# Optimization experiments

Hardware: AMD Instinct MI355X
Metric: run time of the kernel (lower is better)

Reference implementation:

```python
import jax, jax.numpy as jnp
import numpy as np
import math

D, H = 128, 8
B, LC, LQ = 8, 512, 64


def pos_signal(channels, length):
    # tensor2tensor timing signal, returned as [C, L]
    pos = jnp.arange(length, dtype=jnp.float32)
    nts = channels // 2
    inc = math.log(1.0e4) / (nts - 1)
    inv = jnp.exp(jnp.arange(nts, dtype=jnp.float32) * -inc)
    st = pos[:, None] * inv[None, :]                      # [L, nts]
    sig = jnp.concatenate([jnp.sin(st), jnp.cos(st)], 1)  # [L, C]
    return sig.T


def mask_logits(t, m):
    return t * m + (1.0 - m) * -1e30


def ln_c(x, g, b):  # LayerNorm over channel dim of [B, D, L]
    mu = jnp.mean(x, axis=1, keepdims=True)
    var = jnp.mean((x - mu) ** 2, axis=1, keepdims=True)
    return (x - mu) / jnp.sqrt(var + 1e-5) * g[None, :, None] + b[None, :, None]


def conv1x1(x, w, b=None):  # x [B, I, L], w [O, I]
    y = jnp.einsum('oi,bil->bol', w, x)
    return y if b is None else y + b[None, :, None]


def dw_sep_conv(x, dw, pw, pwb):  # depthwise (k, no bias) -> pointwise (bias) -> relu
    k = dw.shape[-1]
    y = jax.lax.conv_general_dilated(x, dw[:, None, :], (1,), [(k // 2, k // 2)],
        dimension_numbers=('NCH', 'OIH', 'NCH'), feature_group_count=x.shape[1])
    return jax.nn.relu(conv1x1(y, pw, pwb))


def self_attention(x, mem_w, q_w, mask, n_head):  # x [B, D, L]
    b, d, L = x.shape
    dh = d // n_head
    mem = jnp.einsum('oi,bil->blo', mem_w, x)  # [B, L, 2D]
    q = jnp.einsum('oi,bil->blo', q_w, x)      # [B, L, D]
    def heads(t):
        return t.reshape(b, L, n_head, dh).transpose(0, 2, 1, 3)  # [B, H, L, dh]
    Qh = heads(q) * dh ** -0.5
    K = heads(mem[..., :d])
    V = heads(mem[..., d:])
    logits = jnp.einsum('bhqe,bhke->bhqk', Qh, K)
    logits = mask_logits(logits, mask[:, None, None, :])
    w = jax.nn.softmax(logits, axis=-1)
    o = jnp.einsum('bhqk,bhke->bhqe', w, V)
    return o.transpose(0, 2, 1, 3).reshape(b, L, d).transpose(0, 2, 1)


def encoder_block(x, mask, p, n_head):
    out = x + pos_signal(x.shape[1], x.shape[2])[None]
    n_conv = p['dw'].shape[0]
    for i in range(n_conv):
        res = out
        out = ln_c(out, p['lnc_g'][i], p['lnc_b'][i])
        out = dw_sep_conv(out, p['dw'][i], p['pw'][i], p['pw_b'][i]) + res
    res = out
    out = ln_c(out, p['ln1_g'], p['ln1_b'])
    out = self_attention(out, p['mem_w'], p['q_w'], mask, n_head) + res
    res = out
    out = ln_c(out, p['ln2_g'], p['ln2_b'])
    out = jax.nn.relu(conv1x1(out, p['ffn1_w'], p['ffn1_b']))
    out = conv1x1(out, p['ffn2_w'], p['ffn2_b'])
    return out + res


def cq_attention(Ce, Qe, cmask, qmask, w4C, w4Q, w4mlu, cq_b):
    Cx = Ce.transpose(0, 2, 1)   # [B, Lc, 2D]
    Qx = Qe.transpose(0, 2, 1)   # [B, Lq, 2D]
    s0 = jnp.einsum('bld,d->bl', Cx, w4C)[:, :, None]
    s1 = jnp.einsum('bqd,d->bq', Qx, w4Q)[:, None, :]
    s2 = jnp.einsum('bld,bqd->blq', Cx * w4mlu[None, None, :], Qx)
    S = s0 + s1 + s2 + cq_b
    S1 = jax.nn.softmax(mask_logits(S, qmask[:, None, :]), axis=2)
    S2 = jax.nn.softmax(mask_logits(S, cmask[:, :, None]), axis=1)
    A = jnp.einsum('blq,bqd->bld', S1, Qx)
    Bt = jnp.einsum('blq,bmq,bmd->bld', S1, S2, Cx)  # (S1 @ S2^T) @ C
    out = jnp.concatenate([Cx, A, Cx * A, Cx * Bt], axis=2)
    return out.transpose(0, 2, 1)  # [B, 8D, Lc]


def _forward(C, Q, maskC, maskQ, e_dw, e_pw, e_pw_b, e_lnc_g, e_lnc_b, e_mem_w, e_q_w,
             e_ffn1_w, e_ffn1_b, e_ffn2_w, e_ffn2_b, e_ln1_g, e_ln1_b, e_ln2_g, e_ln2_b,
             w4C, w4Q, w4mlu, cq_b, resizer_w,
             m_dw, m_pw, m_pw_b, m_lnc_g, m_lnc_b, m_mem_w, m_q_w,
             m_ffn1_w, m_ffn1_b, m_ffn2_w, m_ffn2_b, m_ln1_g, m_ln1_b, m_ln2_g, m_ln2_b):
    ep = dict(dw=e_dw, pw=e_pw, pw_b=e_pw_b, lnc_g=e_lnc_g, lnc_b=e_lnc_b,
              mem_w=e_mem_w, q_w=e_q_w, ffn1_w=e_ffn1_w, ffn1_b=e_ffn1_b,
              ffn2_w=e_ffn2_w, ffn2_b=e_ffn2_b, ln1_g=e_ln1_g, ln1_b=e_ln1_b,
              ln2_g=e_ln2_g, ln2_b=e_ln2_b)
    mp = dict(dw=m_dw, pw=m_pw, pw_b=m_pw_b, lnc_g=m_lnc_g, lnc_b=m_lnc_b,
              mem_w=m_mem_w, q_w=m_q_w, ffn1_w=m_ffn1_w, ffn1_b=m_ffn1_b,
              ffn2_w=m_ffn2_w, ffn2_b=m_ffn2_b, ln1_g=m_ln1_g, ln1_b=m_ln1_b,
              ln2_g=m_ln2_g, ln2_b=m_ln2_b)
    Ce = encoder_block(C, maskC, ep, H)
    Qe = encoder_block(Q, maskQ, ep, H)
    Ce = jnp.concatenate([Ce, C], axis=1)  # encode_fusion -> [B, 2D, Lc]
    Qe = jnp.concatenate([Qe, Q], axis=1)
    X = cq_attention(Ce, Qe, maskC, maskQ, w4C, w4Q, w4mlu, cq_b)
    X = jnp.concatenate([X, Ce], axis=1)   # match_fusion -> [B, 10D, Lc]
    M0 = conv1x1(X, resizer_w)             # [B, D, Lc]

    def run(m):
        def step(carry, p):
            return encoder_block(carry, maskC, p, H), None
        m, _ = jax.lax.scan(step, m, mp)
        return m

    M1 = run(M0)
    M2 = run(M1)
    M3 = run(M2)
    return M1, M2, M3


def setup_inputs() -> dict:
    key = jax.random.key(0)
    ks = iter(jax.random.split(key, 48))
    def rn(shape, scale):
        return jax.random.normal(next(ks), shape, dtype=jnp.float32) * scale
    s1 = 1.0 / math.sqrt(D)
    s2 = 1.0 / math.sqrt(2 * D)
    f32 = jnp.float32
    return dict(
        C=rn((B, D, LC), 1.0), Q=rn((B, D, LQ), 1.0),
        maskC=jnp.ones((B, LC), f32), maskQ=jnp.ones((B, LQ), f32),
        e_dw=rn((4, D, 7), 1.0 / math.sqrt(7)), e_pw=rn((4, D, D), s1),
        e_pw_b=jnp.zeros((4, D), f32), e_lnc_g=jnp.ones((4, D), f32), e_lnc_b=jnp.zeros((4, D), f32),
        e_mem_w=rn((2 * D, D), s1), e_q_w=rn((D, D), s1),
        e_ffn1_w=rn((D, D), s1), e_ffn1_b=jnp.zeros((D,), f32),
        e_ffn2_w=rn((D, D), s1), e_ffn2_b=jnp.zeros((D,), f32),
        e_ln1_g=jnp.ones((D,), f32), e_ln1_b=jnp.zeros((D,), f32),
        e_ln2_g=jnp.ones((D,), f32), e_ln2_b=jnp.zeros((D,), f32),
        w4C=rn((2 * D,), s2), w4Q=rn((2 * D,), s2), w4mlu=rn((2 * D,), s2),
        cq_b=jnp.zeros((1,), f32),
        resizer_w=rn((D, 10 * D), 1.0 / math.sqrt(10 * D)),
        m_dw=rn((7, 2, D, 5), 1.0 / math.sqrt(5)), m_pw=rn((7, 2, D, D), s1),
        m_pw_b=jnp.zeros((7, 2, D), f32), m_lnc_g=jnp.ones((7, 2, D), f32), m_lnc_b=jnp.zeros((7, 2, D), f32),
        m_mem_w=rn((7, 2 * D, D), s1), m_q_w=rn((7, D, D), s1),
        m_ffn1_w=rn((7, D, D), s1), m_ffn1_b=jnp.zeros((7, D), f32),
        m_ffn2_w=rn((7, D, D), s1), m_ffn2_b=jnp.zeros((7, D), f32),
        m_ln1_g=jnp.ones((7, D), f32), m_ln1_b=jnp.zeros((7, D), f32),
        m_ln2_g=jnp.ones((7, D), f32), m_ln2_b=jnp.zeros((7, D), f32),
    )


def reference(C, Q, maskC, maskQ, e_dw, e_pw, e_pw_b, e_lnc_g, e_lnc_b, e_mem_w, e_q_w,
              e_ffn1_w, e_ffn1_b, e_ffn2_w, e_ffn2_b, e_ln1_g, e_ln1_b, e_ln2_g, e_ln2_b,
              w4C, w4Q, w4mlu, cq_b, resizer_w,
              m_dw, m_pw, m_pw_b, m_lnc_g, m_lnc_b, m_mem_w, m_q_w,
              m_ffn1_w, m_ffn1_b, m_ffn2_w, m_ffn2_b, m_ln1_g, m_ln1_b, m_ln2_g, m_ln2_b):
    return _forward(C, Q, maskC, maskQ, e_dw, e_pw, e_pw_b, e_lnc_g, e_lnc_b, e_mem_w, e_q_w,
                    e_ffn1_w, e_ffn1_b, e_ffn2_w, e_ffn2_b, e_ln1_g, e_ln1_b, e_ln2_g, e_ln2_b,
                    w4C, w4Q, w4mlu, cq_b, resizer_w,
                    m_dw, m_pw, m_pw_b, m_lnc_g, m_lnc_b, m_mem_w, m_q_w,
                    m_ffn1_w, m_ffn1_b, m_ffn2_w, m_ffn2_b, m_ln1_g, m_ln1_b, m_ln2_g, m_ln2_b)
```

## Files before the change

kernel.cpp:

```cpp
#include <hip/hip_runtime.h>
#include <math.h>

#define D_  128
#define B_  8
#define H_  8
#define LC_ 512
#define LQ_ 64

typedef float f32x4 __attribute__((ext_vector_type(4)));
typedef short bf16x8 __attribute__((ext_vector_type(8)));
typedef short short4v __attribute__((ext_vector_type(4)));
typedef unsigned short ushortT;

__device__ inline short bfr(float x) {
  unsigned u = __float_as_uint(x);
  u += 0x7fff + ((u >> 16) & 1);
  return (short)(u >> 16);
}
__device__ inline float bfi(ushortT u) {
  return __uint_as_float(((unsigned)u) << 16);
}

__device__ inline bf16x8 mk8(short4v lo, short4v hi) {
  bf16x8 r;
  r[0] = lo[0]; r[1] = lo[1]; r[2] = lo[2]; r[3] = lo[3];
  r[4] = hi[0]; r[5] = hi[1]; r[6] = hi[2]; r[7] = hi[3];
  return r;
}

__device__ inline bf16x8 ldA(const ushortT* row, int koff) {
  short4v lo = *(const short4v*)(row + koff);
  short4v hi = *(const short4v*)(row + koff + 16);
  return mk8(lo, hi);
}
__device__ inline bf16x8 ldB2(const ushortT* plo, const ushortT* phi) {
  short4v lo = *(const short4v*)plo;
  short4v hi = *(const short4v*)phi;
  return mk8(lo, hi);
}

__global__ void k_prep(const float* a0, const float* a1, const float* a2,
                       const float* a3, const float* a4, const float* a5,
                       const float* a6, const float* a7, const float* a8,
                       const float* a9, const float* a10, ushortT* dst) {
  int i = blockIdx.x * 256 + threadIdx.x;
  if (i >= 1114112) return;
  const float* s; int lo;
  if      (i <   65536) { s = a0;  lo = i; }
  else if (i <   98304) { s = a1;  lo = i - 65536; }
  else if (i <  114688) { s = a2;  lo = i - 98304; }
  else if (i <  131072) { s = a3;  lo = i - 114688; }
  else if (i <  147456) { s = a4;  lo = i - 131072; }
  else if (i <  311296) { s = a5;  lo = i - 147456; }
  else if (i <  540672) { s = a6;  lo = i - 311296; }
  else if (i <  770048) { s = a7;  lo = i - 540672; }
  else if (i <  884736) { s = a8;  lo = i - 770048; }
  else if (i <  999424) { s = a9;  lo = i - 884736; }
  else                  { s = a10; lo = i - 999424; }
  dst[i] = (ushortT)bfr(s[lo]);
}

template <int KK, int ADDPOS>
__global__ __launch_bounds__(256) void k_fusedconv(
    const float* __restrict__ x, float* __restrict__ yout,
    const float* __restrict__ dw1, const ushortT* __restrict__ pw1,
    const float* __restrict__ pb1, const float* __restrict__ g1,
    const float* __restrict__ be1,
    const float* __restrict__ dw2, const ushortT* __restrict__ pw2,
    const float* __restrict__ pb2, const float* __restrict__ g2w,
    const float* __restrict__ be2, int L) {
  const int HALO = KK / 2;
  const int W1 = 32 + 2 * HALO;
  __shared__ __align__(16) float raw[128 * 40];
  __shared__ __align__(16) ushortT l1o[128 * 36];
  __shared__ __align__(16) ushortT xbf1[32 * 32 * 4];
  __shared__ float mu1[40], rs1[40], mu2[32], rs2[32], ps[160], psq[160];
  ushortT* xbf2 = (ushortT*)raw;
  int l0 = blockIdx.x * 16;
  int o0 = blockIdx.y * 64;
  int b = blockIdx.z;
  int tid = threadIdx.x;
  for (int idx = tid; idx < 128 * W1; idx += 256) {
    int d = idx / W1, c = idx - d * W1;
    int gl = l0 - 8 - HALO + c;
    float v = 0.f;
    if (gl >= 0 && gl < L) {
      v = x[((size_t)b * 128 + d) * L + gl];
      if (ADDPOS) {
        int j = d & 63;
        float arg = (float)gl * expf(-(float)j * 0.14619588f);
        v += (d < 64) ? sinf(arg) : cosf(arg);
      }
    }
    raw[d * 40 + c] = v;
  }
  __syncthreads();
  if (tid < 4 * W1) {
    int c = tid % W1, hh = tid / W1;
    float s = 0.f, s2 = 0.f;
    for (int d = hh * 32; d < hh * 32 + 32; d++) {
      float v = raw[d * 40 + c];
      s += v; s2 += v * v;
    }
    ps[tid] = s; psq[tid] = s2;
  }
  __syncthreads();
  if (tid < W1) {
    float s = ps[tid] + ps[tid + W1] + ps[tid + 2 * W1] + ps[tid + 3 * W1];
    float s2 = psq[tid] + psq[tid + W1] + psq[tid + 2 * W1] + psq[tid + 3 * W1];
    float mu = s * (1.f / 128.f);
    float var = fmaxf(s2 * (1.f / 128.f) - mu * mu, 0.f);
    mu1[tid] = mu; rs1[tid] = rsqrtf(var + 1e-5f);
  }
  __syncthreads();
  {
    int cc0 = tid & 31, dbase = tid >> 5;
#pragma unroll
    for (int kq = 0; kq < 4; kq++) {
      short4v pk;
#pragma unroll
      for (int e = 0; e < 4; e++) {
        int d = dbase * 16 + kq * 4 + e;
        float gg = g1[d], bb = be1[d];
        const float* wr = dw1 + d * KK;
        float acc = 0.f;
#pragma unroll
        for (int t = 0; t < KK; t++) {
          int ci = cc0 + t;
          int gl = l0 - 8 - HALO + ci;
          float lv = 0.f;
          if (gl >= 0 && gl < L)
            lv = (raw[d * 40 + ci] - mu1[ci]) * rs1[ci] * gg + bb;
          acc += wr[t] * lv;
        }
        pk[e] = bfr(acc);
      }
      *(short4v*)&xbf1[(((dbase * 4 + kq) * 32) + cc0) * 4] = pk;
    }
  }
  __syncthreads();
  int w = tid >> 6, lane = tid & 63, g2 = lane >> 4, r = lane & 15;
  {
    f32x4 acc[2][2];
#pragma unroll
    for (int i = 0; i < 2; i++)
#pragma unroll
      for (int nt = 0; nt < 2; nt++) acc[i][nt] = (f32x4){0.f, 0.f, 0.f, 0.f};
#pragma unroll
    for (int i = 0; i < 2; i++) {
      const ushortT* arow = pw1 + (size_t)((2 * w + i) * 16 + r) * 128;
#pragma unroll
      for (int kk = 0; kk < 4; kk++) {
        bf16x8 a = ldA(arow, kk * 32 + g2 * 4);
#pragma unroll
// ... 318 lines not shown
  int b = blockIdx.z;
  int tid = threadIdx.x;
  int w = tid >> 6;
  int h = w & 7, kh = w >> 3;
  int lane = tid & 63;
  int g2 = lane >> 4, r = lane & 15;
  const float* qb = qp + ((size_t)b * 128 + h * 16) * L;
  const float* kb = memKV + ((size_t)b * 256 + h * 16) * L;
  const float* vb = memKV + ((size_t)b * 256 + 128 + h * 16) * L;
  const float* mk = mask + (size_t)b * L;
  int qcol = q0 + r;
  bf16x8 qf;
#pragma unroll
  for (int j = 0; j < 4; j++)
    qf[j] = bfr(qb[(size_t)(g2 * 4 + j) * L + qcol] * 0.25f);
  qf[4] = 0; qf[5] = 0; qf[6] = 0; qf[7] = 0;
  float m_run = -INFINITY, ssum = 0.f;
  f32x4 O = {0.f, 0.f, 0.f, 0.f};
  int kbeg = kh * (L / 2), kend = (kh + 1) * (L / 2);
  for (int k0 = kbeg; k0 < kend; k0 += NCH * 16) {
    f32x4 sd[NCH];
#pragma unroll
    for (int mc = 0; mc < NCH; mc++) {
      bf16x8 kf;
      int krow = k0 + mc * 16 + r;
#pragma unroll
      for (int j = 0; j < 4; j++)
        kf[j] = bfr(kb[(size_t)(g2 * 4 + j) * L + krow]);
      kf[4] = 0; kf[5] = 0; kf[6] = 0; kf[7] = 0;
      f32x4 z = {0.f, 0.f, 0.f, 0.f};
      sd[mc] = __builtin_amdgcn_mfma_f32_16x16x32_bf16(kf, qf, z, 0, 0, 0);
    }
    float tm = -INFINITY;
#pragma unroll
    for (int mc = 0; mc < NCH; mc++) {
#pragma unroll
      for (int p = 0; p < 4; p++) {
        float mv = mk[k0 + mc * 16 + g2 * 4 + p];
        float sv = sd[mc][p] * mv + (1.f - mv) * (-1e30f);
        sd[mc][p] = sv;
        tm = fmaxf(tm, sv);
      }
    }
    tm = fmaxf(tm, __shfl_xor(tm, 16));
    tm = fmaxf(tm, __shfl_xor(tm, 32));
    float nm = fmaxf(m_run, tm);
    float c = __expf(m_run - nm);
    ssum *= c;
    O[0] *= c; O[1] *= c; O[2] *= c; O[3] *= c;
    float psum = 0.f;
    bf16x8 pf[NCH / 2];
#pragma unroll
    for (int c2 = 0; c2 < NCH / 2; c2++) {
#pragma unroll
      for (int j = 0; j < 4; j++) {
        float e0 = __expf(sd[2 * c2][j] - nm);
        float e1 = __expf(sd[2 * c2 + 1][j] - nm);
        psum += e0 + e1;
        pf[c2][j] = bfr(e0);
        pf[c2][j + 4] = bfr(e1);
      }
    }
    psum += __shfl_xor(psum, 16);
    psum += __shfl_xor(psum, 32);
    ssum += psum;
#pragma unroll
    for (int c2 = 0; c2 < NCH / 2; c2++) {
      const float* vrow = vb + (size_t)r * L + k0 + c2 * 32 + g2 * 4;
      float4 v0 = *(const float4*)vrow;
      float4 v1 = *(const float4*)(vrow + 16);
      bf16x8 vf;
      vf[0] = bfr(v0.x); vf[1] = bfr(v0.y); vf[2] = bfr(v0.z); vf[3] = bfr(v0.w);
      vf[4] = bfr(v1.x); vf[5] = bfr(v1.y); vf[6] = bfr(v1.z); vf[7] = bfr(v1.w);
      O = __builtin_amdgcn_mfma_f32_16x16x32_bf16(vf, pf[c2], O, 0, 0, 0);
    }
    m_run = nm;
  }
  if (kh == 1) {
    msh[h][lane] = m_run;
    ssh[h][lane] = ssum;
#pragma unroll
    for (int p = 0; p < 4; p++) Osh[h][lane][p] = O[p];
  }
  __syncthreads();
  if (kh == 0) {
    float mB = msh[h][lane], sB = ssh[h][lane];
    float nm = fmaxf(m_run, mB);
    float cA = __expf(m_run - nm), cB = __expf(mB - nm);
    float inv = 1.f / (ssum * cA + sB * cB);
#pragma unroll
    for (int p = 0; p < 4; p++) {
      int d = h * 16 + g2 * 4 + p;
      float ov = (O[p] * cA + Osh[h][lane][p] * cB) * inv;
      updT[d * 16 + r] = cur[((size_t)b * 128 + d) * L + qcol] + ov;
    }
  }
  __syncthreads();
  {
    int c = tid & 15, hh = tid >> 4;
    float s = 0.f, s2 = 0.f;
    for (int d = hh * 2; d < hh * 2 + 2; d++) {
      float v = updT[d * 16 + c];
      s += v; s2 += v * v;
    }
    ps[tid] = s; psq[tid] = s2;
  }
  __syncthreads();
  if (tid < 16) {
    float s = 0.f, s2 = 0.f;
    for (int hh = 0; hh < 64; hh++) { s += ps[hh * 16 + tid]; s2 += psq[hh * 16 + tid]; }
    float mu = s * (1.f / 128.f);
    float var = fmaxf(s2 * (1.f / 128.f) - mu * mu, 0.f);
    mu_s[tid] = mu; rs_s[tid] = rsqrtf(var + 1e-5f);
  }
  __syncthreads();
  for (int idx = tid; idx < 2048; idx += 1024) {
    int d = idx >> 4, c = idx & 15;
    float val = (updT[d * 16 + c] - mu_s[c]) * rs_s[c] * g[d] + be[d];
    xbf[(((d >> 2) * 16) + c) * 4 + (d & 3)] = (ushortT)bfr(val);
  }
  __syncthreads();
  if (w < 8) {
    f32x4 acc = {0.f, 0.f, 0.f, 0.f};
    const ushortT* ar = w1bf + (size_t)(16 * w + r) * 128;
#pragma unroll
    for (int kk = 0; kk < 4; kk++) {
      bf16x8 a = ldA(ar, kk * 32 + g2 * 4);
      bf16x8 bb = ldB2(&xbf[(((kk * 8 + g2) * 16) + r) * 4],
                       &xbf[(((kk * 8 + 4 + g2) * 16) + r) * 4]);
      acc = __builtin_amdgcn_mfma_f32_16x16x32_bf16(a, bb, acc, 0, 0, 0);
    }
#pragma unroll
    for (int p = 0; p < 4; p++) {
      int dmid = 16 * w + g2 * 4 + p;
      float val = fmaxf(acc[p] + b1[dmid], 0.f);
      midbf[(((4 * w + g2) * 16) + r) * 4 + p] = (ushortT)bfr(val);
    }
  }
  __syncthreads();
  if (w < 8) {
    f32x4 a2 = {0.f, 0.f, 0.f, 0.f};
    const ushortT* ar = w2bf + (size_t)(16 * w + r) * 128;
#pragma unroll
    for (int kk = 0; kk < 4; kk++) {
      bf16x8 a = ldA(ar, kk * 32 + g2 * 4);
      bf16x8 bb = ldB2(&midbf[(((kk * 8 + g2) * 16) + r) * 4],
                       &midbf[(((kk * 8 + 4 + g2) * 16) + r) * 4]);
      a2 = __builtin_amdgcn_mfma_f32_16x16x32_bf16(a, bb, a2, 0, 0, 0);
    }
#pragma unroll
    for (int p = 0; p < 4; p++) {
      int o = 16 * w + g2 * 4 + p;
      cur[((size_t)b * 128 + o) * L + q0 + r] = a2[p] + b2[o] + updT[o * 16 + r];
    }
  }
}


__global__ void k_concat2(const float* __restrict__ x1, const float* __restrict__ x2,
                          float* __restrict__ out, int L, int total) {
  int idx = blockIdx.x * 256 + threadIdx.x;
  if (idx >= total) return;
  int l = idx % L;
  int c = (idx / L) & 255;
  int b = idx / (L * 256);
  float v = (c < 128) ? x1[((size_t)b * 128 + c) * L + l]
                      : x2[((size_t)b * 128 + (c - 128)) * L + l];
  out[idx] = v;
}

__global__ void k_cqSrow(const float* __restrict__ Ce, const float* __restrict__ Qe,
                         const float* __restrict__ w4C, const float* __restrict__ w4Q,
                         const float* __restrict__ w4mlu, const float* __restrict__ cqb,
                         const float* __restrict__ qmask,
                         float* __restrict__ S, float* __restrict__ S1) {
  int idx = blockIdx.x * 256 + threadIdx.x;
  int q = idx & 63;
  int l = (idx >> 6) % LC_;
  int b = (idx >> 6) / LC_;
  const float* ce = Ce + (size_t)b * 256 * LC_ + l;
  const float* qe = Qe + (size_t)b * 256 * LQ_ + q;
  float acc = 0.f, a0 = 0.f, a1 = 0.f;
#pragma unroll 8
  for (int j = 0; j < 256; j++) {
    float cv = ce[(size_t)j * LC_];
    float qv = qe[(size_t)j * LQ_];
    acc += cv * w4mlu[j] * qv;
    a0 += cv * w4C[j];
    a1 += qv * w4Q[j];
  }
  float sv = acc + a0 + a1 + cqb[0];
  S[idx] = sv;
  float mv = qmask[b * LQ_ + q];
  float v = sv * mv + (1.f - mv) * (-1e30f);
  float mx = v;
  for (int off = 32; off; off >>= 1) mx = fmaxf(mx, __shfl_xor(mx, off));
  float p = expf(v - mx);
  float s = p;
  for (int off = 32; off; off >>= 1) s += __shfl_xor(s, off);
  S1[idx] = p / s;
}

__global__ __launch_bounds__(256) void k_softmax_col(
    const float* __restrict__ S, const float* __restrict__ cmask, float* __restrict__ S2) {
  int q = blockIdx.x & 63, b = blockIdx.x >> 6;
  int tid = threadIdx.x;
  __shared__ float redm[4], reds[4];
  const float* col = S + (size_t)b * LC_ * LQ_ + q;
  const float* mk = cmask + b * LC_;
  float vm[2];
#pragma unroll
  for (int k = 0; k < 2; k++) {
    int l = tid + 256 * k;
    float mv = mk[l];
    vm[k] = col[(size_t)l * LQ_] * mv + (1.f - mv) * (-1e30f);
  }
  float mx = fmaxf(vm[0], vm[1]);
  for (int off = 32; off; off >>= 1) mx = fmaxf(mx, __shfl_xor(mx, off));
  if ((tid & 63) == 0) redm[tid >> 6] = mx;
  __syncthreads();
  mx = fmaxf(fmaxf(redm[0], redm[1]), fmaxf(redm[2], redm[3]));
  float e0 = expf(vm[0] - mx), e1 = expf(vm[1] - mx);
  float s = e0 + e1;
  for (int off = 32; off; off >>= 1) s += __shfl_xor(s, off);
  if ((tid & 63) == 0) reds[tid >> 6] = s;
  __syncthreads();
  float invs = 1.f / (reds[0] + reds[1] + reds[2] + reds[3]);
  float* out = S2 + (size_t)b * LC_ * LQ_ + q;
  out[(size_t)tid * LQ_] = e0 * invs;
  out[(size_t)(tid + 256) * LQ_] = e1 * invs;
}

__global__ void k_cqY(const float* __restrict__ S2, const float* __restrict__ Ce,
                      float* __restrict__ Y) {
  int idx = blockIdx.x * 256 + threadIdx.x;
  if (idx >= B_ * 256 * LQ_) return;
  int q = idx & 63;
  int j = (idx >> 6) & 255;
  int b = idx >> 14;
  const float* s2 = S2 + (size_t)b * LC_ * LQ_ + q;
  const float* ce = Ce + ((size_t)b * 256 + j) * LC_;
  float acc = 0.f;
#pragma unroll 8
  for (int l = 0; l < LC_; l++) acc += s2[(size_t)l * LQ_] * ce[l];
  Y[idx] = acc;
}

__global__ __launch_bounds__(256) void k_cqAB(
    const float* __restrict__ S1, const float* __restrict__ Qe, const float* __restrict__ Y,
    float* __restrict__ A, float* __restrict__ Bt) {
  __shared__ float s1s[64][65];
  int l0 = blockIdx.x * 64;
  int b = blockIdx.z;
  int tid = threadIdx.x;
  for (int idx = tid; idx < 64 * 64; idx += 256) {
    int l = idx >> 6, q = idx & 63;
    s1s[l][q] = S1[((size_t)b * LC_ + l0 + l) * LQ_ + q];
  }
  __syncthreads();
  int ll = tid & 63, jj = tid >> 6;
  int j = blockIdx.y * 4 + jj;
  const float* qe = Qe + ((size_t)b * 256 + j) * LQ_;
  const float* yb = Y + ((size_t)b * 256 + j) * LQ_;
  float a = 0.f, bt = 0.f;
#pragma unroll 8
  for (int q = 0; q < 64; q++) {
    float sv = s1s[ll][q];
    a += sv * qe[q];
    bt += sv * yb[q];
  }
  A[((size_t)b * 256 + j) * LC_ + l0 + ll] = a;
  Bt[((size_t)b * 256 + j) * LC_ + l0 + ll] = bt;
}

__global__ __launch_bounds__(256) void k_resizer_mfma(
    const float* __restrict__ Ce, const float* __restrict__ A,
    const float* __restrict__ Bt, const ushortT* __restrict__ wbf,
    float* __restrict__ y) {
  __shared__ __align__(16) ushortT xbf[16 * 16 * 4];
  int l0 = blockIdx.x * 16;
  int o0 = blockIdx.y * 64;
  int b = blockIdx.z;
  int tid = threadIdx.x;
  int w = tid >> 6, lane = tid & 63, g2 = lane >> 4, r = lane & 15;
  const ushortT* arow = wbf + (size_t)(o0 + 16 * w + r) * 1280;
  f32x4 acc0 = {0.f, 0.f, 0.f, 0.f};
  for (int kt = 0; kt < 1280; kt += 64) {
    __syncthreads();
    for (int idx = tid; idx < 1024; idx += 256) {
      int kloc = idx >> 4, cc = idx & 15;
      int ch = kt + kloc;
      int seg = ch >> 8;
      int j = ch & 255;
      size_t p = ((size_t)b * 256 + j) * LC_ + l0 + cc;
      float v;
      if (seg == 0 || seg == 4) v = Ce[p];
      else if (seg == 1) v = A[p];
      else if (seg == 2) v = Ce[p] * A[p];
      else v = Ce[p] * Bt[p];
      xbf[(((kloc >> 2) * 16) + cc) * 4 + (kloc & 3)] = (ushortT)bfr(v);
    }
    __syncthreads();
#pragma unroll
    for (int kk2 = 0; kk2 < 2; kk2++) {
      bf16x8 a = ldA(arow, kt + kk2 * 32 + g2 * 4);
      bf16x8 b0 = ldB2(&xbf[(((kk2 * 8 + g2) * 16) + r) * 4],
// ... 14 lines not shown
  const float* lnc_g[4]; const float* lnc_b[4];
  const float* dw[4]; const ushortT* pw[4]; const float* pw_b[4];
  const ushortT* mem_w; const ushortT* q_w;
  const float* ln1_g; const float* ln1_b;
  const ushortT* ffn1_w; const float* ffn1_b;
  const ushortT* ffn2_w; const float* ffn2_b;
  const float* ln2_g; const float* ln2_b;
};

static void conv_pair_only(hipStream_t st, const float* in, float* out, int L,
                           const BlkP& P, int i0, bool addpos) {
  dim3 gc(L / 16, 2, B_);
  if (addpos)
    k_fusedconv<7, 1><<<gc, 256, 0, st>>>(in, out,
        P.dw[i0], P.pw[i0], P.pw_b[i0], P.lnc_g[i0], P.lnc_b[i0],
        P.dw[i0+1], P.pw[i0+1], P.pw_b[i0+1], P.lnc_g[i0+1], P.lnc_b[i0+1], L);
  else
    k_fusedconv<7, 0><<<gc, 256, 0, st>>>(in, out,
        P.dw[i0], P.pw[i0], P.pw_b[i0], P.lnc_g[i0], P.lnc_b[i0],
        P.dw[i0+1], P.pw[i0+1], P.pw_b[i0+1], P.lnc_g[i0+1], P.lnc_b[i0+1], L);
}

template <int KK, int ADDPOS>
static void convproj(hipStream_t st, const float* in, float* out, float* mkv,
                     float* qpb, int L, const BlkP& P, int i0) {
  k_convproj<KK, ADDPOS><<<dim3(L / 16, 1, B_), 512, 0, st>>>(in, out,
      P.dw[i0], P.pw[i0], P.pw_b[i0], P.lnc_g[i0], P.lnc_b[i0],
      P.dw[i0+1], P.pw[i0+1], P.pw_b[i0+1], P.lnc_g[i0+1], P.lnc_b[i0+1],
      P.mem_w, P.q_w, P.ln1_g, P.ln1_b, mkv, qpb, L);
}

static void attnffn(hipStream_t st, float* cur, float* mkv, float* qpb,
                    const float* mask, int L, const BlkP& P) {
  if (L == LC_)
    k_attnffn<8><<<dim3(L / 16, 1, B_), 1024, 0, st>>>(mkv, qpb, mask, cur,
        P.ffn1_w, P.ffn1_b, P.ffn2_w, P.ffn2_b, P.ln2_g, P.ln2_b, L);
  else
    k_attnffn<2><<<dim3(L / 16, 1, B_), 1024, 0, st>>>(mkv, qpb, mask, cur,
        P.ffn1_w, P.ffn1_b, P.ffn2_w, P.ffn2_b, P.ln2_g, P.ln2_b, L);
}

extern "C" void kernel_launch(void* const* d_in, const int* in_sizes, int n_in,
                              void* d_out, int out_size, void* d_ws, size_t ws_size,
                              hipStream_t stream) {
  (void)in_sizes; (void)n_in; (void)out_size; (void)ws_size;
  const float* C        = (const float*)d_in[0];
  const float* Q        = (const float*)d_in[1];
  const float* maskC    = (const float*)d_in[2];
  const float* maskQ    = (const float*)d_in[3];
  const float* e_dw     = (const float*)d_in[4];
  const float* e_pw     = (const float*)d_in[5];
  const float* e_pw_b   = (const float*)d_in[6];
  const float* e_lnc_g  = (const float*)d_in[7];
  const float* e_lnc_b  = (const float*)d_in[8];
  const float* e_mem_w  = (const float*)d_in[9];
  const float* e_q_w    = (const float*)d_in[10];
  const float* e_ffn1_w = (const float*)d_in[11];
  const float* e_ffn1_b = (const float*)d_in[12];
  const float* e_ffn2_w = (const float*)d_in[13];
  const float* e_ffn2_b = (const float*)d_in[14];
  const float* e_ln1_g  = (const float*)d_in[15];
  const float* e_ln1_b  = (const float*)d_in[16];
  const float* e_ln2_g  = (const float*)d_in[17];
  const float* e_ln2_b  = (const float*)d_in[18];
  const float* w4C      = (const float*)d_in[19];
  const float* w4Q      = (const float*)d_in[20];
  const float* w4mlu    = (const float*)d_in[21];
  const float* cq_b     = (const float*)d_in[22];
  const float* resizer_w= (const float*)d_in[23];
  const float* m_dw     = (const float*)d_in[24];
  const float* m_pw     = (const float*)d_in[25];
  const float* m_pw_b   = (const float*)d_in[26];
  const float* m_lnc_g  = (const float*)d_in[27];
  const float* m_lnc_b  = (const float*)d_in[28];
  const float* m_mem_w  = (const float*)d_in[29];
  const float* m_q_w    = (const float*)d_in[30];
  const float* m_ffn1_w = (const float*)d_in[31];
  const float* m_ffn1_b = (const float*)d_in[32];
  const float* m_ffn2_w = (const float*)d_in[33];
  const float* m_ffn2_b = (const float*)d_in[34];
  const float* m_ln1_g  = (const float*)d_in[35];
  const float* m_ln1_b  = (const float*)d_in[36];
  const float* m_ln2_g  = (const float*)d_in[37];
  const float* m_ln2_b  = (const float*)d_in[38];

  float* ws = (float*)d_ws;
  const size_t SB = (size_t)B_ * D_ * LC_;
  float* cur  = ws;
  float* aux  = cur + SB;
  float* mkv  = aux + SB;
  float* qpb  = mkv + 2 * SB;
  float* Ce   = qpb + SB;
  float* Qe   = Ce + 2 * SB;
  float* Sbuf = Qe + (size_t)B_ * 256 * LQ_;
  float* S1   = Sbuf + (size_t)B_ * LC_ * LQ_;
  float* S2   = S1 + (size_t)B_ * LC_ * LQ_;
  float* Yb   = S2 + (size_t)B_ * LC_ * LQ_;
  float* Mb   = Yb + (size_t)B_ * 256 * LQ_;
  float* Ab   = mkv;
  float* Bb   = cur;
  ushortT* wb = (ushortT*)(Mb + SB);
  ushortT* w_epw  = wb;
  ushortT* w_emem = wb + 65536;
  ushortT* w_eq   = wb + 98304;
  ushortT* w_ef1  = wb + 114688;
  ushortT* w_ef2  = wb + 131072;
  ushortT* w_rsz  = wb + 147456;
  ushortT* w_mpw  = wb + 311296;
  ushortT* w_mmem = wb + 540672;
  ushortT* w_mq   = wb + 770048;
  ushortT* w_mf1  = wb + 884736;
  ushortT* w_mf2  = wb + 999424;

  k_prep<<<(1114112 + 255) / 256, 256, 0, stream>>>(
      e_pw, e_mem_w, e_q_w, e_ffn1_w, e_ffn2_w, resizer_w,
      m_pw, m_mem_w, m_q_w, m_ffn1_w, m_ffn2_w, wb);

  BlkP ep{};
  ep.k = 7;
  for (int i = 0; i < 4; i++) {
    ep.lnc_g[i] = e_lnc_g + i * 128;
    ep.lnc_b[i] = e_lnc_b + i * 128;
    ep.dw[i]    = e_dw + i * 128 * 7;
    ep.pw[i]    = w_epw + (size_t)i * 128 * 128;
    ep.pw_b[i]  = e_pw_b + i * 128;
  }
  ep.mem_w = w_emem; ep.q_w = w_eq;
  ep.ln1_g = e_ln1_g; ep.ln1_b = e_ln1_b;
  ep.ffn1_w = w_ef1; ep.ffn1_b = e_ffn1_b;
  ep.ffn2_w = w_ef2; ep.ffn2_b = e_ffn2_b;
  ep.ln2_g = e_ln2_g; ep.ln2_b = e_ln2_b;

  conv_pair_only(stream, C, cur, LC_, ep, 0, true);
  convproj<7, 0>(stream, cur, aux, mkv, qpb, LC_, ep, 2);
  attnffn(stream, aux, mkv, qpb, maskC, LC_, ep);
  {
    int tot = B_ * 256 * LC_;
    k_concat2<<<(tot + 255) / 256, 256, 0, stream>>>(aux, C, Ce, LC_, tot);
  }
  conv_pair_only(stream, Q, cur, LQ_, ep, 0, true);
  convproj<7, 0>(stream, cur, aux, mkv, qpb, LQ_, ep, 2);
  attnffn(stream, aux, mkv, qpb, maskQ, LQ_, ep);
  {
    int tot = B_ * 256 * LQ_;
    k_concat2<<<(tot + 255) / 256, 256, 0, stream>>>(aux, Q, Qe, LQ_, tot);
  }

  k_cqSrow<<<(B_ * LC_ * LQ_) / 256, 256, 0, stream>>>(Ce, Qe, w4C, w4Q, w4mlu, cq_b, maskQ, Sbuf, S1);
  k_softmax_col<<<B_ * LQ_, 256, 0, stream>>>(Sbuf, maskC, S2);
  k_cqY<<<(B_ * 256 * LQ_) / 256, 256, 0, stream>>>(S2, Ce, Yb);
  k_cqAB<<<dim3(LC_ / 64, 64, B_), 256, 0, stream>>>(S1, Qe, Yb, Ab, Bb);
  k_resizer_mfma<<<dim3(LC_ / 16, 2, B_), 256, 0, stream>>>(Ce, Ab, Bb, w_rsz, Mb);

  float* out = (float*)d_out;
  float* bufs[2] = {cur, aux};
  int cb = 0;
  const float* src = Mb;
  for (int r = 0; r < 3; r++) {
    for (int bi = 0; bi < 7; bi++) {
      BlkP mp{};
      mp.k = 5;
      for (int ci = 0; ci < 2; ci++) {
        int pc = bi * 2 + ci;
        mp.lnc_g[ci] = m_lnc_g + pc * 128;
        mp.lnc_b[ci] = m_lnc_b + pc * 128;
        mp.dw[ci]    = m_dw + pc * 128 * 5;
        mp.pw[ci]    = w_mpw + (size_t)pc * 128 * 128;
        mp.pw_b[ci]  = m_pw_b + pc * 128;
      }
      mp.mem_w  = w_mmem + (size_t)bi * 256 * 128;
      mp.q_w    = w_mq + (size_t)bi * 128 * 128;
      mp.ffn1_w = w_mf1 + (size_t)bi * 128 * 128;
      mp.ffn1_b = m_ffn1_b + bi * 128;
      mp.ffn2_w = w_mf2 + (size_t)bi * 128 * 128;
      mp.ffn2_b = m_ffn2_b + bi * 128;
      mp.ln1_g = m_ln1_g + bi * 128; mp.ln1_b = m_ln1_b + bi * 128;
      mp.ln2_g = m_ln2_g + bi * 128; mp.ln2_b = m_ln2_b + bi * 128;
      float* ob = bufs[cb];
      convproj<5, 1>(stream, src, ob, mkv, qpb, LC_, mp, 0);
      attnffn(stream, ob, mkv, qpb, maskC, LC_, mp);
      src = ob;
      cb ^= 1;
    }
    hipMemcpyAsync(out + (size_t)r * SB, src, SB * sizeof(float),
                   hipMemcpyDeviceToDevice, stream);
  }
}
```

Baseline: 1.441 ms.

## Fuse model encoder stack into one persistent cooperative kernel with grid syncs

Result: slower. 2.808 ms (+94.9%).

```diff
diff --git a/kernel.cpp b/kernel.cpp
--- a/kernel.cpp
+++ b/kernel.cpp
@@ -1,5 +1,8 @@
 #include <hip/hip_runtime.h>
+#include <hip/hip_cooperative_groups.h>
 #include <math.h>
+
+namespace cg = cooperative_groups;
 
 #define D_  128
 #define B_  8
@@ -624,6 +627,449 @@
     for (int p = 0; p < 4; p++) {
       int o = 16 * w + g2 * 4 + p;
       cur[((size_t)b * 128 + o) * L + q0 + r] = a2[p] + b2[o] + updT[o * 16 + r];
+    }
+  }
+}
+
+struct MArgs {
+  const float* maskC;
+  float* mkv; float* qpb;
+  const float* Mb; float* cur; float* aux; float* out;
+  const float* m_dw; const ushortT* w_mpw; const float* m_pw_b;
+  const float* m_lnc_g; const float* m_lnc_b;
+  const ushortT* w_mmem; const ushortT* w_mq;
+  const ushortT* w_mf1; const float* m_ffn1_b;
+  const ushortT* w_mf2; const float* m_ffn2_b;
+  const float* m_ln1_g; const float* m_ln1_b;
+  const float* m_ln2_g; const float* m_ln2_b;
+};
+
+__device__ __forceinline__ void conv_phase(
+    char* smem, const float* x, float* yout,
+    const float* dw1, const ushortT* pw1, const float* pb1,
+    const float* g1, const float* be1,
+    const float* dw2, const ushortT* pw2, const float* pb2,
+    const float* g2w, const float* be2,
+    const ushortT* memw, const ushortT* qw,
+    const float* g3, const float* be3,
+    float* mkv, float* qp, int l0, int b, int tid) {
+  const int KK = 5, HALO = 2, W1 = 36, L = LC_;
+  float* raw = (float*)smem;
+  ushortT* l1o = (ushortT*)(smem + 20480);
+  ushortT* xbf1 = (ushortT*)(smem + 29696);
+  ushortT* c2o = (ushortT*)(smem + 37888);
+  float* mu1 = (float*)(smem + 41984);
+  float* rs1 = (float*)(smem + 42144);
+  float* mu2 = (float*)(smem + 42304);
+  float* rs2 = (float*)(smem + 42432);
+  float* mu3 = (float*)(smem + 42560);
+  float* rs3 = (float*)(smem + 42624);
+  float* ps  = (float*)(smem + 42688);
+  float* psq = (float*)(smem + 46784);
+  ushortT* xbf2 = (ushortT*)raw;
+  ushortT* xbf3 = (ushortT*)(raw + 4096);
+  for (int idx = tid; idx < 128 * W1; idx += 1024) {
+    int d = idx / W1, c = idx - d * W1;
+    int gl = l0 - 8 - HALO + c;
+    float v = 0.f;
+    if (gl >= 0 && gl < L) {
+      v = x[((size_t)b * 128 + d) * L + gl];
+      int j = d & 63;
+      float arg = (float)gl * expf(-(float)j * 0.14619588f);
+      v += (d < 64) ? sinf(arg) : cosf(arg);
+    }
+    raw[d * 40 + c] = v;
+  }
+  __syncthreads();
+  if (tid < 4 * W1) {
+    int c = tid % W1, hh = tid / W1;
+    float s = 0.f, s2 = 0.f;
+    for (int d = hh * 32; d < hh * 32 + 32; d++) {
+      float v = raw[d * 40 + c];
+      s += v; s2 += v * v;
+    }
+    ps[tid] = s; psq[tid] = s2;
+  }
+  __syncthreads();
+  if (tid < W1) {
+    float s = ps[tid] + ps[tid + W1] + ps[tid + 2 * W1] + ps[tid + 3 * W1];
+    float s2 = psq[tid] + psq[tid + W1] + psq[tid + 2 * W1] + psq[tid + 3 * W1];
+    float mu = s * (1.f / 128.f);
+    float var = fmaxf(s2 * (1.f / 128.f) - mu * mu, 0.f);
+    mu1[tid] = mu; rs1[tid] = rsqrtf(var + 1e-5f);
+  }
+  __syncthreads();
+  {
+    int cc0 = tid & 31, dbase = tid >> 5;
+    short4v pk;
+#pragma unroll
+    for (int e = 0; e < 4; e++) {
+      int d = dbase * 4 + e;
+      float gg = g1[d], bb = be1[d];
+      const float* wr = dw1 + d * KK;
+      float acc = 0.f;
+#pragma unroll
+      for (int t = 0; t < KK; t++) {
+        int ci = cc0 + t;
+        int gl = l0 - 8 - HALO + ci;
+        float lv = 0.f;
+        if (gl >= 0 && gl < L)
+          lv = (raw[d * 40 + ci] - mu1[ci]) * rs1[ci] * gg + bb;
+        acc += wr[t] * lv;
+      }
+      pk[e] = bfr(acc);
+    }
+    *(short4v*)&xbf1[((dbase * 32) + cc0) * 4] = pk;
+  }
+  __syncthreads();
+  int w = tid >> 6, lane = tid & 63, g2 = lane >> 4, r = lane & 15;
+  {
+    int m = w & 7, nt = w >> 3;
+    f32x4 acc = {0.f, 0.f, 0.f, 0.f};
+    const ushortT* arow = pw1 + (size_t)(m * 16 + r) * 128;
+#pragma unroll
+    for (int kk = 0; kk < 4; kk++) {
+      bf16x8 a = ldA(arow, kk * 32 + g2 * 4);
+      bf16x8 bb = ldB2(&xbf1[(((kk * 8 + g2) * 32) + nt * 16 + r) * 4],
+                       &xbf1[(((kk * 8 + 4 + g2) * 32) + nt * 16 + r) * 4]);
+      acc = __builtin_amdgcn_mfma_f32_16x16x32_bf16(a, bb, acc, 0, 0, 0);
+    }
+#pragma unroll
+    for (int p = 0; p < 4; p++) {
+      int o = m * 16 + g2 * 4 + p;
+      int c1 = nt * 16 + r;
+      int gl = l0 - 8 + c1;
+      float val = 0.f;
+      if (gl >= 0 && gl < L)
+        val = fmaxf(acc[p] + pb1[o], 0.f) + raw[o * 40 + c1 + HALO];
+      l1o[o * 36 + c1] = (ushortT)bfr(val);
+    }
+  }
+  __syncthreads();
+  if (tid < 128) {
+    int c = tid & 31, hh = tid >> 5;
+    float s = 0.f, s2 = 0.f;
+    for (int d = hh * 32; d < hh * 32 + 32; d++) {
+      float v = bfi(l1o[d * 36 + c]);
+      s += v; s2 += v * v;
+    }
+    ps[tid] = s; psq[tid] = s2;
+  }
+  __syncthreads();
+  if (tid < 32) {
+    float s = ps[tid] + ps[tid + 32] + ps[tid + 64] + ps[tid + 96];
+    float s2 = psq[tid] + psq[tid + 32] + psq[tid + 64] + psq[tid + 96];
+    float mu = s * (1.f / 128.f);
+    float var = fmaxf(s2 * (1.f / 128.f) - mu * mu, 0.f);
+    mu2[tid] = mu; rs2[tid] = rsqrtf(var + 1e-5f);
+  }
+  __syncthreads();
+  {
+    int cc2 = tid & 15, db2 = tid >> 4;
+#pragma unroll
+    for (int e = 0; e < 2; e++) {
+      int d = db2 * 2 + e;
+      float gg = g2w[d], bb = be2[d];
+      const float* wr = dw2 + d * KK;
+      float acc = 0.f;
+#pragma unroll
+      for (int t = 0; t < KK; t++) {
+        int c1 = cc2 + 8 + t - HALO;
+        int gl = l0 + cc2 + t - HALO;
+        float lv = 0.f;
+        if (gl >= 0 && gl < L)
+          lv = (bfi(l1o[d * 36 + c1]) - mu2[c1]) * rs2[c1] * gg + bb;
+        acc += wr[t] * lv;
+      }
+      xbf2[(((d >> 2) * 16) + cc2) * 4 + (d & 3)] = (ushortT)bfr(acc);
+    }
+  }
+  __syncthreads();
+  if (w < 8) {
+    f32x4 a2 = {0.f, 0.f, 0.f, 0.f};
+    const ushortT* arow = pw2 + (size_t)(w * 16 + r) * 128;
+#pragma unroll
+    for (int kk = 0; kk < 4; kk++) {
+      bf16x8 a = ldA(arow, kk * 32 + g2 * 4);
+      bf16x8 bb = ldB2(&xbf2[(((kk * 8 + g2) * 16) + r) * 4],
+                       &xbf2[(((kk * 8 + 4 + g2) * 16) + r) * 4]);
+      a2 = __builtin_amdgcn_mfma_f32_16x16x32_bf16(a, bb, a2, 0, 0, 0);
+    }
+#pragma unroll
+    for (int p = 0; p < 4; p++) {
+      int o = w * 16 + g2 * 4 + p;
+      float val = fmaxf(a2[p] + pb2[o], 0.f) + bfi(l1o[o * 36 + 8 + r]);
+      yout[((size_t)b * 128 + o) * L + l0 + r] = val;
+      c2o[o * 16 + r] = (ushortT)bfr(val);
+    }
+  }
+  __syncthreads();
+  if (tid < 128) {
+    int c = tid & 15, hh = tid >> 4;
+    float s = 0.f, s2 = 0.f;
+    for (int d = hh * 16; d < hh * 16 + 16; d++) {
+      float v = bfi(c2o[d * 16 + c]);
+      s += v; s2 += v * v;
+    }
+    ps[tid] = s; psq[tid] = s2;
+  }
+  __syncthreads();
+  if (tid < 16) {
+    float s = 0.f, s2 = 0.f;
+#pragma unroll
+    for (int hh = 0; hh < 8; hh++) { s += ps[hh * 16 + tid]; s2 += psq[hh * 16 + tid]; }
+    float mu = s * (1.f / 128.f);
+    float var = fmaxf(s2 * (1.f / 128.f) - mu * mu, 0.f);
+    mu3[tid] = mu; rs3[tid] = rsqrtf(var + 1e-5f);
+  }
+  __syncthreads();
+  for (int idx = tid; idx < 2048; idx += 1024) {
+    int d = idx >> 4, c = idx & 15;
+    float val = (bfi(c2o[d * 16 + c]) - mu3[c]) * rs3[c] * g3[d] + be3[d];
+    xbf3[(((d >> 2) * 16) + c) * 4 + (d & 3)] = (ushortT)bfr(val);
+  }
+  __syncthreads();
+#pragma unroll
+  for (int t = 0; t < 2; t++) {
+    int mt = w + 16 * t;
+    if (mt < 24) {
+      const ushortT* arow; float* outp; int obase, O;
+      if (mt < 16) { arow = memw + (size_t)(mt * 16 + r) * 128; outp = mkv; obase = mt * 16; O = 256; }
+      else         { arow = qw + (size_t)((mt - 16) * 16 + r) * 128; outp = qp; obase = (mt - 16) * 16; O = 128; }
+      f32x4 acc = {0.f, 0.f, 0.f, 0.f};
+#pragma unroll
+      for (int kk = 0; kk < 4; kk++) {
+        bf16x8 a = ldA(arow, kk * 32 + g2 * 4);
+        bf16x8 bb = ldB2(&xbf3[(((kk * 8 + g2) * 16) + r) * 4],
+                         &xbf3[(((kk * 8 + 4 + g2) * 16) + r) * 4]);
+        acc = __builtin_amdgcn_mfma_f32_16x16x32_bf16(a, bb, acc, 0, 0, 0);
+      }
+#pragma unroll
+      for (int p = 0; p < 4; p++)
+        outp[((size_t)b * O + obase + g2 * 4 + p) * L + l0 + r] = acc[p];
+    }
+  }
+}
+
+__device__ __forceinline__ void attn_phase(
+    char* smem, const float* memKV, const float* qp, const float* mask,
+    float* cur, const ushortT* w1bf, const float* b1,
+    const ushortT* w2bf, const float* b2,
+    const float* g, const float* be, int q0, int b, int tid) {
+  const int NCH = 8, L = LC_;
+  float* msh = (float*)smem;
+  float* ssh = (float*)(smem + 2048);
+  float* OshF = (float*)(smem + 4096);
+  float* updT = (float*)(smem + 12288);
+  ushortT* xbf = (ushortT*)(smem + 20480);
+  ushortT* midbf = (ushortT*)(smem + 24576);
+  float* mu_s = (float*)(smem + 28672);
+  float* rs_s = (float*)(smem + 28736);
+  float* ps = (float*)(smem + 28800);
+  float* psq = (float*)(smem + 32896);
+  int w = tid >> 6;
+  int h = w & 7, kh = w >> 3;
+  int lane = tid & 63;
+  int g2 = lane >> 4, r = lane & 15;
+  const float* qb = qp + ((size_t)b * 128 + h * 16) * L;
+  const float* kb = memKV + ((size_t)b * 256 + h * 16) * L;
+  const float* vb = memKV + ((size_t)b * 256 + 128 + h * 16) * L;
+  const float* mk = mask + (size_t)b * L;
+  int qcol = q0 + r;
+  bf16x8 qf;
+#pragma unroll
+  for (int j = 0; j < 4; j++)
+    qf[j] = bfr(qb[(size_t)(g2 * 4 + j) * L + qcol] * 0.25f);
+  qf[4] = 0; qf[5] = 0; qf[6] = 0; qf[7] = 0;
+  float m_run = -INFINITY, ssum = 0.f;
+  f32x4 O = {0.f, 0.f, 0.f, 0.f};
+  int kbeg = kh * (L / 2), kend = (kh + 1) * (L / 2);
+  for (int k0 = kbeg; k0 < kend; k0 += NCH * 16) {
+    f32x4 sd[NCH];
+#pragma unroll
+    for (int mc = 0; mc < NCH; mc++) {
+      bf16x8 kf;
+      int krow = k0 + mc * 16 + r;
+#pragma unroll
+      for (int j = 0; j < 4; j++)
+        kf[j] = bfr(kb[(size_t)(g2 * 4 + j) * L + krow]);
+      kf[4] = 0; kf[5] = 0; kf[6] = 0; kf[7] = 0;
+      f32x4 z = {0.f, 0.f, 0.f, 0.f};
+      sd[mc] = __builtin_amdgcn_mfma_f32_16x16x32_bf16(kf, qf, z, 0, 0, 0);
+    }
+    float tm = -INFINITY;
+#pragma unroll
+    for (int mc = 0; mc < NCH; mc++) {
+#pragma unroll
+      for (int p = 0; p < 4; p++) {
+        float mv = mk[k0 + mc * 16 + g2 * 4 + p];
+        float sv = sd[mc][p] * mv + (1.f - mv) * (-1e30f);
+        sd[mc][p] = sv;
+        tm = fmaxf(tm, sv);
+      }
+    }
+    tm = fmaxf(tm, __shfl_xor(tm, 16));
+    tm = fmaxf(tm, __shfl_xor(tm, 32));
+    float nm = fmaxf(m_run, tm);
+    float c = __expf(m_run - nm);
+    ssum *= c;
+    O[0] *= c; O[1] *= c; O[2] *= c; O[3] *= c;
+    float psum = 0.f;
+    bf16x8 pf[NCH / 2];
+#pragma unroll
+    for (int c2 = 0; c2 < NCH / 2; c2++) {
+#pragma unroll
+      for (int j = 0; j < 4; j++) {
+        float e0 = __expf(sd[2 * c2][j] - nm);
+        float e1 = __expf(sd[2 * c2 + 1][j] - nm);
+        psum += e0 + e1;
+        pf[c2][j] = bfr(e0);
+        pf[c2][j + 4] = bfr(e1);
+      }
+    }
+    psum += __shfl_xor(psum, 16);
+    psum += __shfl_xor(psum, 32);
+    ssum += psum;
+#pragma unroll
+    for (int c2 = 0; c2 < NCH / 2; c2++) {
+      const float* vrow = vb + (size_t)r * L + k0 + c2 * 32 + g2 * 4;
+      float4 v0 = *(const float4*)vrow;
+      float4 v1 = *(const float4*)(vrow + 16);
+      bf16x8 vf;
+      vf[0] = bfr(v0.x); vf[1] = bfr(v0.y); vf[2] = bfr(v0.z); vf[3] = bfr(v0.w);
+      vf[4] = bfr(v1.x); vf[5] = bfr(v1.y); vf[6] = bfr(v1.z); vf[7] = bfr(v1.w);
+      O = __builtin_amdgcn_mfma_f32_16x16x32_bf16(vf, pf[c2], O, 0, 0, 0);
+    }
+    m_run = nm;
+  }
+  if (kh == 1) {
+    msh[h * 64 + lane] = m_run;
+    ssh[h * 64 + lane] = ssum;
+#pragma unroll
+    for (int p = 0; p < 4; p++) OshF[(h * 64 + lane) * 4 + p] = O[p];
+  }
+  __syncthreads();
+  if (kh == 0) {
+    float mB = msh[h * 64 + lane], sB = ssh[h * 64 + lane];
+    float nm = fmaxf(m_run, mB);
+    float cA = __expf(m_run - nm), cB = __expf(mB - nm);
+    float inv = 1.f / (ssum * cA + sB * cB);
+#pragma unroll
+    for (int p = 0; p < 4; p++) {
+      int d = h * 16 + g2 * 4 + p;
+      float ov = (O[p] * cA + OshF[(h * 64 + lane) * 4 + p] * cB) * inv;
+      updT[d * 16 + r] = cur[((size_t)b * 128 + d) * L + qcol] + ov;
+    }
+  }
+  __syncthreads();
+  {
+    int c = tid & 15, hh = tid >> 4;
+    float s = 0.f, s2 = 0.f;
+    for (int d = hh * 2; d < hh * 2 + 2; d++) {
+      float v = updT[d * 16 + c];
+      s += v; s2 += v * v;
+    }
+    ps[tid] = s; psq[tid] = s2;
+  }
+  __syncthreads();
+  if (tid < 16) {
+    float s = 0.f, s2 = 0.f;
+    for (int hh = 0; hh < 64; hh++) { s += ps[hh * 16 + tid]; s2 += psq[hh * 16 + tid]; }
+    float mu = s * (1.f / 128.f);
+    float var = fmaxf(s2 * (1.f / 128.f) - mu * mu, 0.f);
+    mu_s[tid] = mu; rs_s[tid] = rsqrtf(var + 1e-5f);
+  }
+  __syncthreads();
+  for (int idx = tid; idx < 2048; idx += 1024) {
+    int d = idx >> 4, c = idx & 15;
+    float val = (updT[d * 16 + c] - mu_s[c]) * rs_s[c] * g[d] + be[d];
+    xbf[(((d >> 2) * 16) + c) * 4 + (d & 3)] = (ushortT)bfr(val);
+  }
+  __syncthreads();
+  if (w < 8) {
+    f32x4 acc = {0.f, 0.f, 0.f, 0.f};
+    const ushortT* ar = w1bf + (size_t)(16 * w + r) * 128;
+#pragma unroll
+    for (int kk = 0; kk < 4; kk++) {
+      bf16x8 a = ldA(ar, kk * 32 + g2 * 4);
+      bf16x8 bb = ldB2(&xbf[(((kk * 8 + g2) * 16) + r) * 4],
+                       &xbf[(((kk * 8 + 4 + g2) * 16) + r) * 4]);
+      acc = __builtin_amdgcn_mfma_f32_16x16x32_bf16(a, bb, acc, 0, 0, 0);
+    }
+#pragma unroll
+    for (int p = 0; p < 4; p++) {
+      int dmid = 16 * w + g2 * 4 + p;
+      float val = fmaxf(acc[p] + b1[dmid], 0.f);
+      midbf[(((4 * w + g2) * 16) + r) * 4 + p] = (ushortT)bfr(val);
+    }
+  }
+  __syncthreads();
+  if (w < 8) {
+    f32x4 a2 = {0.f, 0.f, 0.f, 0.f};
+    const ushortT* ar = w2bf + (size_t)(16 * w + r) * 128;
+#pragma unroll
+    for (int kk = 0; kk < 4; kk++) {
+      bf16x8 a = ldA(ar, kk * 32 + g2 * 4);
+      bf16x8 bb = ldB2(&midbf[(((kk * 8 + g2) * 16) + r) * 4],
+                       &midbf[(((kk * 8 + 4 + g2) * 16) + r) * 4]);
+      a2 = __builtin_amdgcn_mfma_f32_16x16x32_bf16(a, bb, a2, 0, 0, 0);
+    }
+#pragma unroll
+    for (int p = 0; p < 4; p++) {
+      int o = 16 * w + g2 * 4 + p;
+      cur[((size_t)b * 128 + o) * L + q0 + r] = a2[p] + b2[o] + updT[o * 16 + r];
+    }
+  }
+}
+
+__global__ __launch_bounds__(1024, 4) void k_model(MArgs A) {
+  __shared__ __align__(16) char smem[50880];
+  cg::grid_group gg = cg::this_grid();
+  int tid = threadIdx.x;
+  int bx = blockIdx.x;
+  int b = bx >> 5, lt = bx & 31;
+  int l0 = lt * 16;
+  const size_t SB = (size_t)B_ * D_ * LC_;
+  const float* src = A.Mb;
+  float* pa = A.cur;
+  float* pb = A.aux;
+  for (int r = 0; r < 3; r++) {
+    for (int bi = 0; bi < 7; bi++) {
+      int pc0 = bi * 2, pc1 = bi * 2 + 1;
+      const float* dw1 = A.m_dw + (size_t)pc0 * 640;
+      const float* dw2 = A.m_dw + (size_t)pc1 * 640;
+      const ushortT* pw1 = A.w_mpw + (size_t)pc0 * 16384;
+      const ushortT* pw2 = A.w_mpw + (size_t)pc1 * 16384;
+      const float* pb1 = A.m_pw_b + pc0 * 128;
+      const float* pb2 = A.m_pw_b + pc1 * 128;
+      const float* g1 = A.m_lnc_g + pc0 * 128;
+      const float* be1 = A.m_lnc_b + pc0 * 128;
+      const float* g2w = A.m_lnc_g + pc1 * 128;
+      const float* be2 = A.m_lnc_b + pc1 * 128;
+      const ushortT* memw = A.w_mmem + (size_t)bi * 32768;
+      const ushortT* qw = A.w_mq + (size_t)bi * 16384;
+      const float* g3 = A.m_ln1_g + bi * 128;
+      const float* be3 = A.m_ln1_b + bi * 128;
+      const ushortT* f1 = A.w_mf1 + (size_t)bi * 16384;
+      const float* b1 = A.m_ffn1_b + bi * 128;
+      const ushortT* f2 = A.w_mf2 + (size_t)bi * 16384;
+      const float* b2 = A.m_ffn2_b + bi * 128;
+      const float* gL = A.m_ln2_g + bi * 128;
+      const float* beL = A.m_ln2_b + bi * 128;
+      float* ob = pa;
+      conv_phase(smem, src, ob, dw1, pw1, pb1, g1, be1, dw2, pw2, pb2, g2w, be2,
+                 memw, qw, g3, be3, A.mkv, A.qpb, l0, b, tid);
+      gg.sync();
+      attn_phase(smem, A.mkv, A.qpb, A.maskC, ob, f1, b1, f2, b2, gL, beL,
+                 l0, b, tid);
+      gg.sync();
+      src = ob;
+      float* t = pa; pa = pb; pb = t;
+    }
+    {
+      size_t off = (size_t)bx * 2048 + tid * 2;
+      float2 v = *(const float2*)&src[off];
+      *(float2*)&A.out[(size_t)r * SB + off] = v;
     }
   }
 }
@@ -944,37 +1390,17 @@
   k_cqAB<<<dim3(LC_ / 64, 64, B_), 256, 0, stream>>>(S1, Qe, Yb, Ab, Bb);
   k_resizer_mfma<<<dim3(LC_ / 16, 2, B_), 256, 0, stream>>>(Ce, Ab, Bb, w_rsz, Mb);
 
-  float* out = (float*)d_out;
-  float* bufs[2] = {cur, aux};
-  int cb = 0;
-  const float* src = Mb;
-  for (int r = 0; r < 3; r++) {
-    for (int bi = 0; bi < 7; bi++) {
-      BlkP mp{};
-      mp.k = 5;
-      for (int ci = 0; ci < 2; ci++) {
-        int pc = bi * 2 + ci;
-        mp.lnc_g[ci] = m_lnc_g + pc * 128;
-        mp.lnc_b[ci] = m_lnc_b + pc * 128;
-        mp.dw[ci]    = m_dw + pc * 128 * 5;
-        mp.pw[ci]    = w_mpw + (size_t)pc * 128 * 128;
-        mp.pw_b[ci]  = m_pw_b + pc * 128;
-      }
-      mp.mem_w  = w_mmem + (size_t)bi * 256 * 128;
-      mp.q_w    = w_mq + (size_t)bi * 128 * 128;
-      mp.ffn1_w = w_mf1 + (size_t)bi * 128 * 128;
-      mp.ffn1_b = m_ffn1_b + bi * 128;
-      mp.ffn2_w = w_mf2 + (size_t)bi * 128 * 128;
-      mp.ffn2_b = m_ffn2_b + bi * 128;
-      mp.ln1_g = m_ln1_g + bi * 128; mp.ln1_b = m_ln1_b + bi * 128;
-      mp.ln2_g = m_ln2_g + bi * 128; mp.ln2_b = m_ln2_b + bi * 128;
-      float* ob = bufs[cb];
-      convproj<5, 1>(stream, src, ob, mkv, qpb, LC_, mp, 0);
-      attnffn(stream, ob, mkv, qpb, maskC, LC_, mp);
-      src = ob;
-      cb ^= 1;
-    }
-    hipMemcpyAsync(out + (size_t)r * SB, src, SB * sizeof(float),
-                   hipMemcpyDeviceToDevice, stream);
-  }
-}
+  MArgs ma;
+  ma.maskC = maskC;
+  ma.mkv = mkv; ma.qpb = qpb;
+  ma.Mb = Mb; ma.cur = cur; ma.aux = aux; ma.out = (float*)d_out;
+  ma.m_dw = m_dw; ma.w_mpw = w_mpw; ma.m_pw_b = m_pw_b;
+  ma.m_lnc_g = m_lnc_g; ma.m_lnc_b = m_lnc_b;
+  ma.w_mmem = w_mmem; ma.w_mq = w_mq;
+  ma.w_mf1 = w_mf1; ma.m_ffn1_b = m_ffn1_b;
+  ma.w_mf2 = w_mf2; ma.m_ffn2_b = m_ffn2_b;
+  ma.m_ln1_g = m_ln1_g; ma.m_ln1_b = m_ln1_b;
+  ma.m_ln2_g = m_ln2_g; ma.m_ln2_b = m_ln2_b;
+  void* kargs[] = {&ma};
+  hipLaunchCooperativeKernel((void*)k_model, dim3(256), dim3(1024), kargs, 0, stream);
+}
```
